# Optimization experiments

Hardware: AMD Instinct MI355X
Metric: run time of the kernel (lower is better)

The kernel has to match this reference:

```python
import jax, jax.numpy as jnp
import numpy as np

B, DIM, L = 16, 1024, 1024
EPS = 1e-12  # F.normalize eps


def l2norm(x, axis=1):
    # torch F.normalize: x / clamp_min(||x||_2, eps)
    n = jnp.sqrt(jnp.sum(x * x, axis=axis, keepdims=True))
    return x / jnp.maximum(n, EPS)


def setup_inputs() -> dict:
    key = jax.random.key(0)
    ks = jax.random.split(key, 8)
    inp = {
        "V": jax.random.normal(ks[0], (B, DIM, L), dtype=jnp.float32),
        "T": jax.random.normal(ks[1], (B, DIM, L), dtype=jnp.float32),
    }
    scale = 1.0 / np.sqrt(DIM)
    names = ["WQ1", "WK1", "WV1", "Wq2", "Wk2", "Wv2"]
    for i, nme in enumerate(names):
        inp[nme] = jax.random.normal(ks[2 + i], (DIM, DIM), dtype=jnp.float32) * scale
    return inp


def reference(V, T, WQ1, WK1, WV1, Wq2, Wk2, Wv2):
    # V, T: [B, dim, L]
    T = l2norm(T, axis=1)                      # normalize over feature dim
    Vt = jnp.swapaxes(V, -2, -1)               # [B, L, dim]
    Tt = jnp.swapaxes(T, -2, -1)               # [B, L, dim]

    relu = jax.nn.relu
    q1 = relu(jnp.einsum('bld,ed->ble', Vt, WQ1))
    k1 = relu(jnp.einsum('bld,ed->ble', Tt, WK1))
    v1 = relu(jnp.einsum('bld,ed->ble', Tt, WV1))
    q2 = relu(jnp.einsum('bld,ed->ble', Tt, Wq2))
    k2 = relu(jnp.einsum('bld,ed->ble', Vt, Wk2))
    v2 = relu(jnp.einsum('bld,ed->ble', Vt, Wv2))

    inv_sqrt_d = 1.0 / jnp.sqrt(jnp.asarray(DIM, dtype=q1.dtype))

    s1 = jnp.einsum('bqd,bkd->bqk', q1, k1) * inv_sqrt_d   # [B, Lv, Lt]
    p1 = jax.nn.softmax(s1, axis=1)                        # softmax over query axis (dim=1)
    w1 = jnp.einsum('bqk,bkd->bqd', p1, v1)                # [B, Lv, dim]
    cV = l2norm(V + jnp.swapaxes(w1, -2, -1), axis=1)      # [B, dim, Lv]

    s2 = jnp.einsum('bqd,bkd->bqk', q2, k2) * inv_sqrt_d   # [B, Lt, Lv]
    p2 = jax.nn.softmax(s2, axis=1)
    w2 = jnp.einsum('bqk,bkd->bqd', p2, v2)                # [B, Lt, dim]
    cT = l2norm(T + jnp.swapaxes(w2, -2, -1), axis=1)      # [B, dim, Lt]

    return l2norm(cV + cT, axis=1)
```

## Files before the change

kernel.cpp:

```cpp
#include <hip/hip_runtime.h>

#define L 1024
#define DIM 1024
#define NB 16

typedef unsigned short u16;
typedef __attribute__((ext_vector_type(4))) float f32x4;
typedef __attribute__((ext_vector_type(8))) short s16x8;

__device__ __forceinline__ float bf2f(u16 x){
  union { unsigned u; float f; } c; c.u = ((unsigned)x) << 16; return c.f;
}
__device__ __forceinline__ u16 f2bf(float f){
  union { float f; unsigned u; } c; c.f = f;
  unsigned r = c.u + 0x7fffu + ((c.u >> 16) & 1u);
  return (u16)(r >> 16);
}
__device__ __forceinline__ void gload_lds16(const void* g, void* l){
  __builtin_amdgcn_global_load_lds(
      (const __attribute__((address_space(1))) void*)g,
      (__attribute__((address_space(3))) void*)l, 16, 0, 0);
}

struct WPtrs { const float* p[6]; };

__global__ __launch_bounds__(256) void k_wconv(WPtrs wp, u16* out){
  long idx = (long)blockIdx.x * blockDim.x + threadIdx.x;
  long base = idx * 4;
  int w = (int)(base >> 20);
  long off = base & ((1 << 20) - 1);
  float4 v = *(const float4*)(wp.p[w] + off);
  ushort4 o;
  o.x = f2bf(v.x); o.y = f2bf(v.y); o.z = f2bf(v.z); o.w = f2bf(v.w);
  *(ushort4*)(out + base) = o;
}

__global__ __launch_bounds__(256) void k_transpose(const float* X, u16* Xt, int bo){
  __shared__ u16 tile[64][68];
  int b = blockIdx.y;
  int d0 = (blockIdx.x >> 4) * 64;
  int l0 = (blockIdx.x & 15) * 64;
  const float* Xb = X + (long)(bo + b) * DIM * L;
  u16* Xtb = Xt + (long)b * L * DIM;
  int q = threadIdx.x & 15, g = threadIdx.x >> 4;
  for (int r = g; r < 64; r += 16){
    float4 v = *(const float4*)(Xb + (long)(d0 + r) * L + l0 + q * 4);
    ushort4 h; h.x = f2bf(v.x); h.y = f2bf(v.y); h.z = f2bf(v.z); h.w = f2bf(v.w);
    *(ushort4*)&tile[r][q * 4] = h;
  }
  __syncthreads();
  for (int r = g; r < 64; r += 16){
    ushort4 h;
    h.x = tile[q * 4 + 0][r]; h.y = tile[q * 4 + 1][r];
    h.z = tile[q * 4 + 2][r]; h.w = tile[q * 4 + 3][r];
    *(ushort4*)&Xtb[(long)(l0 + r) * DIM + d0 + q * 4] = h;
  }
}

__global__ __launch_bounds__(256) void k_tnorm(const float* T_, u16* Tnt, float* rT, int bo){
  __shared__ float red[16][16][5];
  __shared__ float rn[64];
  __shared__ u16 tile[64][68];
  int b = blockIdx.y; int l0 = blockIdx.x * 64;
  const float* Tb = T_ + (long)(bo + b) * DIM * L;
  int q = threadIdx.x & 15, g = threadIdx.x >> 4;
  f32x4 ss = {0.f, 0.f, 0.f, 0.f};
  for (int d = g; d < DIM; d += 16){
    float4 v = *(const float4*)(Tb + (long)d * L + l0 + q * 4);
    f32x4 vv = {v.x, v.y, v.z, v.w};
    ss += vv * vv;
  }
  #pragma unroll
  for (int e = 0; e < 4; e++) red[g][q][e] = ss[e];
  __syncthreads();
  if (threadIdx.x < 64){
    int c = threadIdx.x;
    float n = 0.f;
    #pragma unroll
    for (int gg = 0; gg < 16; gg++) n += red[gg][c >> 2][c & 3];
    float r = 1.0f / fmaxf(sqrtf(n), 1e-12f);
    rn[c] = r;
    rT[(long)b * L + l0 + c] = r;
  }
  __syncthreads();
  float r0 = rn[q * 4], r1 = rn[q * 4 + 1], r2 = rn[q * 4 + 2], r3 = rn[q * 4 + 3];
  u16* Tntb = Tnt + (long)b * L * DIM;
  for (int ch = 0; ch < 16; ch++){
    int dbase = ch * 64;
    for (int r = g; r < 64; r += 16){
      float4 v = *(const float4*)(Tb + (long)(dbase + r) * L + l0 + q * 4);
      ushort4 h;
      h.x = f2bf(v.x * r0); h.y = f2bf(v.y * r1);
      h.z = f2bf(v.z * r2); h.w = f2bf(v.w * r3);
      *(ushort4*)&tile[r][q * 4] = h;
    }
    __syncthreads();
    for (int r = g; r < 64; r += 16){
      ushort4 h;
      h.x = tile[q * 4 + 0][r]; h.y = tile[q * 4 + 1][r];
      h.z = tile[q * 4 + 2][r]; h.w = tile[q * 4 + 3][r];
      *(ushort4*)&Tntb[(long)(l0 + r) * DIM + dbase + q * 4] = h;
    }
    __syncthreads();
  }
}


struct GemmDesc {
  const u16* A[4]; const u16* B[4]; u16* C[4];
  long sA[4], sB[4], sC[4];
  int epi[4];
  float scale;
};

#define PH(slot, mq, nq, LA, LB, STAGE, WAITC) do {                           \
  if (LA){                                                                    \
    _Pragma("unroll")                                                         \
    for (int f = 0; f < 4; f++){                                              \
      av[f][0] = *(const s16x8*)&lds[(slot)*16384 + arow + (mq)*4096 + f*1024 + cko0]; \
      av[f][1] = *(const s16x8*)&lds[(slot)*16384 + arow + (mq)*4096 + f*1024 + cko1]; \
    }                                                                         \
  }                                                                           \
  if (LB){                                                                    \
    _Pragma("unroll")                                                         \
    for (int g2 = 0; g2 < 2; g2++){                                           \
      bv[nq][g2][0] = *(const s16x8*)&lds[32768 + (slot)*16384 + brow + (nq)*2048 + g2*1024 + cko0]; \
      bv[nq][g2][1] = *(const s16x8*)&lds[32768 + (slot)*16384 + brow + (nq)*2048 + g2*1024 + cko1]; \
    }                                                                         \
  }                                                                           \
  STAGE;                                                                      \
  WAITC;                                                                      \
  __builtin_amdgcn_s_barrier();                                               \
  asm volatile("s_waitcnt lgkmcnt(0)" ::: "memory");                          \
  __builtin_amdgcn_sched_barrier(0);                                          \
  __builtin_amdgcn_s_setprio(1);                                              \
  _Pragma("unroll")                                                           \
  for (int f = 0; f < 4; f++)                                                 \
    _Pragma("unroll")                                                         \
    for (int g2 = 0; g2 < 2; g2++){                                           \
      acc[(mq)*4+f][(nq)*2+g2] = __builtin_amdgcn_mfma_f32_16x16x32_bf16(     \
          av[f][0], bv[nq][g2][0], acc[(mq)*4+f][(nq)*2+g2], 0, 0, 0);        \
      acc[(mq)*4+f][(nq)*2+g2] = __builtin_amdgcn_mfma_f32_16x16x32_bf16(     \
          av[f][1], bv[nq][g2][1], acc[(mq)*4+f][(nq)*2+g2], 0, 0, 0);        \
    }                                                                         \
  __builtin_amdgcn_s_setprio(0);                                              \
  __builtin_amdgcn_s_barrier();                                               \
} while(0)

__global__ __launch_bounds__(512, 2) void k_gemmM(GemmDesc gd, int shift){
  constexpr int K = 1024, NN = 1024, NT = K / 64, NIT = NT / 2;
  __shared__ u16 lds[65536];

  int tid = threadIdx.x;
  int w = tid >> 6, l = tid & 63;
  int wr = w >> 2, wc = w & 3;
  int lr = l & 15, cb = l >> 4;

  int nwg = gridDim.x, cpx = nwg >> 3;
  int swz = (blockIdx.x & 7) * cpx + (blockIdx.x >> 3);
  int mat = swz >> shift;
  int local = swz & ((1 << shift) - 1);
  int batch = local >> 4;
  int tile = local & 15;
  int bm = (tile >> 2) * 256, bn = (tile & 3) * 256;

  const u16* Ab = gd.A[mat] + (long)batch * gd.sA[mat] + (long)bm * K;
  const u16* Bb = gd.B[mat] + (long)batch * gd.sB[mat] + (long)bn * K;
  int epi = gd.epi[mat];

  int arow = (wr * 128 + lr) * 64;
  int brow = (wc * 64 + lr) * 64;
  int cko0 = ((cb) ^ (lr & 7)) * 8;
  int cko1 = ((4 + cb) ^ (lr & 7)) * 8;

  int srow8 = l >> 3;
  int schunk = (l & 7) ^ (l >> 3);

  auto stA = [&](int slot, int t, int q){
    #pragma unroll
    for (int j = 0; j < 2; j++){
      int wb = w * 2 + j;
      int gr = ((wb >> 3) * 128) + ((wb & 7) * 8) + q * 64;
      gload_lds16(Ab + (long)(gr + srow8) * K + t * 64 + schunk * 8,
                  (u16*)lds + slot * 16384 + gr * 64);
    }
  };
  auto stB = [&](int slot, int t, int q){
    #pragma unroll
    for (int j = 0; j < 2; j++){
      int wb = w * 2 + j;
      int gr = ((wb >> 2) * 64) + ((wb & 3) * 8) + q * 32;
      gload_lds16(Bb + (long)(gr + srow8) * K + t * 64 + schunk * 8,
                  (u16*)lds + 32768 + slot * 16384 + gr * 64);
    }
  };

  f32x4 acc[8][4] = {};
  s16x8 av[4][2];
  s16x8 bv[2][2][2];

  stA(0, 0, 0); stB(0, 0, 0); stA(0, 0, 1); stB(0, 0, 1);
  stA(1, 1, 0); stB(1, 1, 0);
  asm volatile("s_waitcnt vmcnt(4)" ::: "memory");
  __builtin_amdgcn_s_barrier();

  #pragma unroll 1
  for (int i = 0; i < NIT - 1; ++i){
    int t1 = 2 * i + 1, t2 = 2 * i + 2, t3 = 2 * i + 3;
    PH(0, 0, 0, 1, 1, stA(1, t1, 1), (void)0);
    PH(0, 0, 1, 0, 1, stB(1, t1, 1), (void)0);
    PH(0, 1, 0, 1, 0, stA(0, t2, 0), (void)0);
    PH(0, 1, 1, 0, 0, stB(0, t2, 0), asm volatile("s_waitcnt vmcnt(4)" ::: "memory"));
    PH(1, 0, 0, 1, 1, stA(0, t2, 1), (void)0);
    PH(1, 0, 1, 0, 1, stB(0, t2, 1), (void)0);
    PH(1, 1, 0, 1, 0, stA(1, t3, 0), (void)0);
    PH(1, 1, 1, 0, 0, stB(1, t3, 0), asm volatile("s_waitcnt vmcnt(4)" ::: "memory"));
  }
  {
    int t1 = NT - 1;
    PH(0, 0, 0, 1, 1, stA(1, t1, 1), (void)0);
    PH(0, 0, 1, 0, 1, stB(1, t1, 1), (void)0);
    PH(0, 1, 0, 1, 0, (void)0, (void)0);
    PH(0, 1, 1, 0, 0, (void)0, asm volatile("s_waitcnt vmcnt(0)" ::: "memory"));
    PH(1, 0, 0, 1, 1, (void)0, (void)0);
    PH(1, 0, 1, 0, 1, (void)0, (void)0);
    PH(1, 1, 0, 1, 0, (void)0, (void)0);
    PH(1, 1, 1, 0, 0, (void)0, (void)0);
  }

  u16* Cb = gd.C[mat] + (long)batch * gd.sC[mat];
  float sc = gd.scale;
  int cb4 = cb * 4;
  #pragma unroll
  for (int ai = 0; ai < 8; ai++)
    #pragma unroll
    for (int j = 0; j < 4; j++)
      #pragma unroll
      for (int r = 0; r < 4; r++){
        float v = acc[ai][j][r];
        if (epi == 0) v = fmaxf(v, 0.f);
        else if (epi == 1) v = __expf(v * sc);
        int row = bm + wr * 128 + ai * 16 + cb4 + r;
        int col = bn + wc * 64 + j * 16 + lr;
        Cb[(long)row * NN + col] = f2bf(v);
      }
}

__global__ __launch_bounds__(256) void k_colsum(const u16* E1, const u16* E2,
                                                float* iz1, float* iz2){
  __shared__ float red[32][8][9];
  int side = blockIdx.x >> 4;
  int k0 = (blockIdx.x & 15) * 64;
  int b = blockIdx.y;
  const u16* Eb = (side ? E2 : E1) + (long)b * L * L + k0;
  float* izp = (side ? iz2 : iz1) + (long)b * L + k0;
  int co = threadIdx.x & 7, g = threadIdx.x >> 3;
  float z[8] = {0.f, 0.f, 0.f, 0.f, 0.f, 0.f, 0.f, 0.f};
  for (int qq = g; qq < L; qq += 32){
    s16x8 h = *(const s16x8*)(Eb + (long)qq * L + co * 8);
    #pragma unroll
    for (int e = 0; e < 8; e++) z[e] += bf2f((u16)h[e]);
  }
  #pragma unroll
  for (int e = 0; e < 8; e++) red[g][co][e] = z[e];
  __syncthreads();
  if (threadIdx.x < 64){
    int c = threadIdx.x;
    float s = 0.f;
    #pragma unroll
    for (int gg = 0; gg < 32; gg++) s += red[gg][c >> 3][c & 7];
    izp[c] = 1.0f / s;
  }
}

__global__ __launch_bounds__(256) void k_zapply(u16* v1, u16* v2,
                                                const float* iz1, const float* iz2){
  int side = blockIdx.y;
  u16* v = side ? v2 : v1;
  const float* izp = side ? iz2 : iz1;
  long base = ((long)blockIdx.x * 256 + threadIdx.x) * 8;
  int batch = (int)(base >> 20);
  int k = (int)(base & 1023);
  s16x8 h = *(const s16x8*)(v + base);
  const float* z = izp + (long)batch * 1024 + k;
  float4 z0 = *(const float4*)z;
  float4 z1 = *(const float4*)(z + 4);
  s16x8 o;
  o[0] = (short)f2bf(bf2f((u16)h[0]) * z0.x);
  o[1] = (short)f2bf(bf2f((u16)h[1]) * z0.y);
  o[2] = (short)f2bf(bf2f((u16)h[2]) * z0.z);
  o[3] = (short)f2bf(bf2f((u16)h[3]) * z0.w);
  o[4] = (short)f2bf(bf2f((u16)h[4]) * z1.x);
  o[5] = (short)f2bf(bf2f((u16)h[5]) * z1.y);
  o[6] = (short)f2bf(bf2f((u16)h[6]) * z1.z);
  o[7] = (short)f2bf(bf2f((u16)h[7]) * z1.w);
  *(s16x8*)(v + base) = o;
}

__global__ __launch_bounds__(1024) void k_final(const float* V, const float* T_,
                                                const float* rT, const u16* w1t,
                                                const u16* w2t, float* out, int bo){
  __shared__ float red[64][16][13];
  __shared__ float fac[3][64];
  int b = blockIdx.y;
  int c0 = blockIdx.x * 64;
  long gbase = (long)(bo + b) * DIM * L + c0;
  long lbase = (long)b * DIM * L + c0;
  int cq = threadIdx.x & 15, g = threadIdx.x >> 4;
  int coff = cq * 4;
  float4 rt4 = *(const float4*)(rT + (long)b * L + c0 + coff);
  f32x4 rtv = {rt4.x, rt4.y, rt4.z, rt4.w};
  f32x4 s1 = {0.f,0.f,0.f,0.f}, s2 = {0.f,0.f,0.f,0.f}, s12 = {0.f,0.f,0.f,0.f};
  for (int d = g; d < DIM; d += 64){
    long o = (long)d * L + coff;
    float4 v = *(const float4*)(V + gbase + o);
    float4 t = *(const float4*)(T_ + gbase + o);
    ushort4 w1 = *(const ushort4*)(w1t + lbase + o);
    ushort4 w2 = *(const ushort4*)(w2t + lbase + o);
    f32x4 a = {v.x + bf2f(w1.x), v.y + bf2f(w1.y), v.z + bf2f(w1.z), v.w + bf2f(w1.w)};
    f32x4 tt = {t.x, t.y, t.z, t.w};
    f32x4 bb = tt * rtv;
    bb[0] += bf2f(w2.x); bb[1] += bf2f(w2.y); bb[2] += bf2f(w2.z); bb[3] += bf2f(w2.w);
    s1 += a * a; s2 += bb * bb; s12 += a * bb;
  }
  #pragma unroll
  for (int e = 0; e < 4; e++){
    red[g][cq][e] = s1[e];
    red[g][cq][4 + e] = s2[e];
    red[g][cq][8 + e] = s12[e];
  }
  __syncthreads();
  if (threadIdx.x < 192){
    int q = threadIdx.x / 12, s = threadIdx.x % 12;
    float acc = 0.f;
    #pragma unroll 8
    for (int gg = 0; gg < 64; gg++) acc += red[gg][q][s];
    red[0][q][s] = acc;
  }
  __syncthreads();
  if (threadIdx.x < 64){
    int c = threadIdx.x;
    float n1 = red[0][c >> 2][c & 3];
    float n2 = red[0][c >> 2][4 + (c & 3)];
    float cc = red[0][c >> 2][8 + (c & 3)];
    float rn1 = 1.f / fmaxf(sqrtf(n1), 1e-12f);
    float rn2 = 1.f / fmaxf(sqrtf(n2), 1e-12f);
    float n3 = n1 * rn1 * rn1 + 2.f * cc * rn1 * rn2 + n2 * rn2 * rn2;
    float rn3 = 1.f / fmaxf(sqrtf(n3), 1e-12f);
    fac[0][c] = rn1; fac[1][c] = rn2; fac[2][c] = rn3;
  }
  __syncthreads();
  f32x4 f1, f2, f3;
  #pragma unroll
  for (int e = 0; e < 4; e++){
    f1[e] = fac[0][coff + e]; f2[e] = fac[1][coff + e]; f3[e] = fac[2][coff + e];
  }
  for (int d = g; d < DIM; d += 64){
    long o = (long)d * L + coff;
    float4 v = *(const float4*)(V + gbase + o);
    float4 t = *(const float4*)(T_ + gbase + o);
    ushort4 w1 = *(const ushort4*)(w1t + lbase + o);
    ushort4 w2 = *(const ushort4*)(w2t + lbase + o);
    f32x4 a = {v.x + bf2f(w1.x), v.y + bf2f(w1.y), v.z + bf2f(w1.z), v.w + bf2f(w1.w)};
    f32x4 tt = {t.x, t.y, t.z, t.w};
    f32x4 bb = tt * rtv;
    bb[0] += bf2f(w2.x); bb[1] += bf2f(w2.y); bb[2] += bf2f(w2.z); bb[3] += bf2f(w2.w);
    f32x4 r = (a * f1 + bb * f2) * f3;
    float4 st = {r[0], r[1], r[2], r[3]};
    *(float4*)(out + gbase + o) = st;
  }
}

extern "C" void kernel_launch(void* const* d_in, const int* in_sizes, int n_in,
                              void* d_out, int out_size, void* d_ws, size_t ws_size,
                              hipStream_t stream) {
  const float* V = (const float*)d_in[0];
  const float* T = (const float*)d_in[1];
  char* ws = (char*)d_ws;
  const long MB = 1 << 20;
  float* out = (float*)d_out;

  int G = NB;
  while (G > 1 && (size_t)((13 + 24 * (long)G) * MB) > ws_size) G >>= 1;
  int shift = 4 + (31 - __builtin_clz((unsigned)G));

  u16*   Wb  = (u16*)(ws);
  float* rT  = (float*)(ws + 12 * MB);
  float* iz1 = (float*)(ws + 12 * MB + 256 * 1024);
  float* iz2 = (float*)(ws + 12 * MB + 512 * 1024);
  char*  bufs = ws + 13 * MB;
  long   BUF  = (long)G * 2 * MB;
  u16* Vt  = (u16*)(bufs + 0  * BUF);
  u16* Tnt = (u16*)(bufs + 1  * BUF);
  u16* q1  = (u16*)(bufs + 2  * BUF);
  u16* k1  = (u16*)(bufs + 3  * BUF);
  u16* q2  = (u16*)(bufs + 4  * BUF);
  u16* k2  = (u16*)(bufs + 5  * BUF);
  u16* E1  = (u16*)(bufs + 6  * BUF);
  u16* E2  = (u16*)(bufs + 7  * BUF);
  u16* v1  = (u16*)(bufs + 8  * BUF);
  u16* v2  = (u16*)(bufs + 9  * BUF);
  u16* w1b = (u16*)(bufs + 10 * BUF);
  u16* w2b = (u16*)(bufs + 11 * BUF);

  WPtrs wp;
  for (int i = 0; i < 6; i++) wp.p[i] = (const float*)d_in[2 + i];
  const u16* WQ1 = Wb + 0L * MB; const u16* WK1 = Wb + 1L * MB;
  const u16* WV1 = Wb + 2L * MB; const u16* Wq2 = Wb + 3L * MB;
  const u16* Wk2 = Wb + 4L * MB; const u16* Wv2 = Wb + 5L * MB;

  long LD = (long)L * DIM;
  const float invsq = 0.03125f;

  GemmDesc g1;
  g1.A[0] = Vt;  g1.B[0] = WQ1; g1.C[0] = q1;
  g1.A[1] = Tnt; g1.B[1] = WK1; g1.C[1] = k1;
  g1.A[2] = Tnt; g1.B[2] = Wq2; g1.C[2] = q2;
  g1.A[3] = Vt;  g1.B[3] = Wk2; g1.C[3] = k2;
  for (int i = 0; i < 4; i++){ g1.sA[i] = LD; g1.sB[i] = 0; g1.sC[i] = LD; g1.epi[i] = 0; }
  g1.scale = 0.f;

  GemmDesc g2;
  g2.A[0] = q1;  g2.B[0] = k1;  g2.C[0] = E1; g2.sA[0] = LD; g2.sB[0] = LD; g2.sC[0] = LD; g2.epi[0] = 1;
  g2.A[1] = q2;  g2.B[1] = k2;  g2.C[1] = E2; g2.sA[1] = LD; g2.sB[1] = LD; g2.sC[1] = LD; g2.epi[1] = 1;
  g2.A[2] = WV1; g2.B[2] = Tnt; g2.C[2] = v1; g2.sA[2] = 0;  g2.sB[2] = LD; g2.sC[2] = LD; g2.epi[2] = 0;
  g2.A[3] = Wv2; g2.B[3] = Vt;  g2.C[3] = v2; g2.sA[3] = 0;  g2.sB[3] = LD; g2.sC[3] = LD; g2.epi[3] = 0;
  g2.scale = invsq;

  GemmDesc g3;
  g3.A[0] = v1; g3.B[0] = E1; g3.C[0] = w1b;
  g3.A[1] = v2; g3.B[1] = E2; g3.C[1] = w2b;
  g3.A[2] = v1; g3.B[2] = E1; g3.C[2] = w1b;
  g3.A[3] = v1; g3.B[3] = E1; g3.C[3] = w1b;
  for (int i = 0; i < 4; i++){ g3.sA[i] = LD; g3.sB[i] = LD; g3.sC[i] = LD; g3.epi[i] = 3; }
  g3.scale = 0.f;

  k_wconv<<<6144, 256, 0, stream>>>(wp, Wb);

  for (int bo = 0; bo < NB; bo += G){
    k_transpose<<<dim3(256, G), 256, 0, stream>>>(V, Vt, bo);
    k_tnorm<<<dim3(16, G), 256, 0, stream>>>(T, Tnt, rT, bo);

    k_gemmM<<<4 * 16 * G, 512, 0, stream>>>(g1, shift);
    k_gemmM<<<4 * 16 * G, 512, 0, stream>>>(g2, shift);
    k_colsum<<<dim3(32, G), 256, 0, stream>>>(E1, E2, iz1, iz2);
    k_zapply<<<dim3(G * 512, 2), 256, 0, stream>>>(v1, v2, iz1, iz2);
    k_gemmM<<<2 * 16 * G, 512, 0, stream>>>(g3, shift);

    k_final<<<dim3(16, G), 1024, 0, stream>>>(V, T, rT, w1b, w2b, out, bo);
  }
}
```

Measured before the change: 654.5 us.

## Reuse workspace buffers via liveness aliasing and fuse column-sum with value scaling

Replaces the twelve per-batch workspace buffers with seven aliased slots. GEMM launches are regrouped (T-side projections, then V-side projections, then each score GEMM alone) so that dead buffers can be overwritten, which lets a larger batch group G fit in the workspace. The column-sum kernel now also rescales v1/v2 by the inverse sums, removing the separate zapply launch and its global round trip for the inverse sums. The final kernel's loops are unrolled by 4. In exchange there are more, smaller GEMM launches, and correctness depends on the aliasing order being right.

```diff
diff --git a/kernel.cpp b/kernel.cpp
--- a/kernel.cpp
+++ b/kernel.cpp
@@ -246,14 +246,15 @@
       }
 }
 
-__global__ __launch_bounds__(256) void k_colsum(const u16* E1, const u16* E2,
-                                                float* iz1, float* iz2){
+__global__ __launch_bounds__(256) void k_colzs(const u16* E1, const u16* E2,
+                                               u16* v1, u16* v2){
   __shared__ float red[32][8][9];
+  __shared__ float invs[64];
   int side = blockIdx.x >> 4;
   int k0 = (blockIdx.x & 15) * 64;
   int b = blockIdx.y;
   const u16* Eb = (side ? E2 : E1) + (long)b * L * L + k0;
-  float* izp = (side ? iz2 : iz1) + (long)b * L + k0;
+  u16* vb = (side ? v2 : v1) + (long)b * L * DIM + k0;
   int co = threadIdx.x & 7, g = threadIdx.x >> 3;
   float z[8] = {0.f, 0.f, 0.f, 0.f, 0.f, 0.f, 0.f, 0.f};
   for (int qq = g; qq < L; qq += 32){
@@ -269,32 +270,19 @@
     float s = 0.f;
     #pragma unroll
     for (int gg = 0; gg < 32; gg++) s += red[gg][c >> 3][c & 7];
-    izp[c] = 1.0f / s;
-  }
-}
-
-__global__ __launch_bounds__(256) void k_zapply(u16* v1, u16* v2,
-                                                const float* iz1, const float* iz2){
-  int side = blockIdx.y;
-  u16* v = side ? v2 : v1;
-  const float* izp = side ? iz2 : iz1;
-  long base = ((long)blockIdx.x * 256 + threadIdx.x) * 8;
-  int batch = (int)(base >> 20);
-  int k = (int)(base & 1023);
-  s16x8 h = *(const s16x8*)(v + base);
-  const float* z = izp + (long)batch * 1024 + k;
-  float4 z0 = *(const float4*)z;
-  float4 z1 = *(const float4*)(z + 4);
-  s16x8 o;
-  o[0] = (short)f2bf(bf2f((u16)h[0]) * z0.x);
-  o[1] = (short)f2bf(bf2f((u16)h[1]) * z0.y);
-  o[2] = (short)f2bf(bf2f((u16)h[2]) * z0.z);
-  o[3] = (short)f2bf(bf2f((u16)h[3]) * z0.w);
-  o[4] = (short)f2bf(bf2f((u16)h[4]) * z1.x);
-  o[5] = (short)f2bf(bf2f((u16)h[5]) * z1.y);
-  o[6] = (short)f2bf(bf2f((u16)h[6]) * z1.z);
-  o[7] = (short)f2bf(bf2f((u16)h[7]) * z1.w);
-  *(s16x8*)(v + base) = o;
+    invs[c] = 1.0f / s;
+  }
+  __syncthreads();
+  float iz[8];
+  #pragma unroll
+  for (int e = 0; e < 8; e++) iz[e] = invs[co * 8 + e];
+  for (int r = g; r < DIM; r += 32){
+    s16x8 h = *(const s16x8*)(vb + (long)r * L + co * 8);
+    s16x8 o;
+    #pragma unroll
+    for (int e = 0; e < 8; e++) o[e] = (short)f2bf(bf2f((u16)h[e]) * iz[e]);
+    *(s16x8*)(vb + (long)r * L + co * 8) = o;
+  }
 }
 
 __global__ __launch_bounds__(1024) void k_final(const float* V, const float* T_,
@@ -311,6 +299,7 @@
   float4 rt4 = *(const float4*)(rT + (long)b * L + c0 + coff);
   f32x4 rtv = {rt4.x, rt4.y, rt4.z, rt4.w};
   f32x4 s1 = {0.f,0.f,0.f,0.f}, s2 = {0.f,0.f,0.f,0.f}, s12 = {0.f,0.f,0.f,0.f};
+  #pragma unroll 4
   for (int d = g; d < DIM; d += 64){
     long o = (long)d * L + coff;
     float4 v = *(const float4*)(V + gbase + o);
@@ -355,6 +344,7 @@
   for (int e = 0; e < 4; e++){
     f1[e] = fac[0][coff + e]; f2[e] = fac[1][coff + e]; f3[e] = fac[2][coff + e];
   }
+  #pragma unroll 4
   for (int d = g; d < DIM; d += 64){
     long o = (long)d * L + coff;
     float4 v = *(const float4*)(V + gbase + o);
@@ -381,27 +371,20 @@
   float* out = (float*)d_out;
 
   int G = NB;
-  while (G > 1 && (size_t)((13 + 24 * (long)G) * MB) > ws_size) G >>= 1;
+  while (G > 1 && (size_t)((13 + 14 * (long)G) * MB) > ws_size) G >>= 1;
   int shift = 4 + (31 - __builtin_clz((unsigned)G));
 
   u16*   Wb  = (u16*)(ws);
   float* rT  = (float*)(ws + 12 * MB);
-  float* iz1 = (float*)(ws + 12 * MB + 256 * 1024);
-  float* iz2 = (float*)(ws + 12 * MB + 512 * 1024);
   char*  bufs = ws + 13 * MB;
   long   BUF  = (long)G * 2 * MB;
-  u16* Vt  = (u16*)(bufs + 0  * BUF);
-  u16* Tnt = (u16*)(bufs + 1  * BUF);
-  u16* q1  = (u16*)(bufs + 2  * BUF);
-  u16* k1  = (u16*)(bufs + 3  * BUF);
-  u16* q2  = (u16*)(bufs + 4  * BUF);
-  u16* k2  = (u16*)(bufs + 5  * BUF);
-  u16* E1  = (u16*)(bufs + 6  * BUF);
-  u16* E2  = (u16*)(bufs + 7  * BUF);
-  u16* v1  = (u16*)(bufs + 8  * BUF);
-  u16* v2  = (u16*)(bufs + 9  * BUF);
-  u16* w1b = (u16*)(bufs + 10 * BUF);
-  u16* w2b = (u16*)(bufs + 11 * BUF);
+  u16* S0 = (u16*)(bufs + 0 * BUF);
+  u16* S1 = (u16*)(bufs + 1 * BUF);
+  u16* S2 = (u16*)(bufs + 2 * BUF);
+  u16* S3 = (u16*)(bufs + 3 * BUF);
+  u16* S4 = (u16*)(bufs + 4 * BUF);
+  u16* S5 = (u16*)(bufs + 5 * BUF);
+  u16* S6 = (u16*)(bufs + 6 * BUF);
 
   WPtrs wp;
   for (int i = 0; i < 6; i++) wp.p[i] = (const float*)d_in[2 + i];
@@ -412,28 +395,42 @@
   long LD = (long)L * DIM;
   const float invsq = 0.03125f;
 
-  GemmDesc g1;
-  g1.A[0] = Vt;  g1.B[0] = WQ1; g1.C[0] = q1;
-  g1.A[1] = Tnt; g1.B[1] = WK1; g1.C[1] = k1;
-  g1.A[2] = Tnt; g1.B[2] = Wq2; g1.C[2] = q2;
-  g1.A[3] = Vt;  g1.B[3] = Wk2; g1.C[3] = k2;
-  for (int i = 0; i < 4; i++){ g1.sA[i] = LD; g1.sB[i] = 0; g1.sC[i] = LD; g1.epi[i] = 0; }
-  g1.scale = 0.f;
-
-  GemmDesc g2;
-  g2.A[0] = q1;  g2.B[0] = k1;  g2.C[0] = E1; g2.sA[0] = LD; g2.sB[0] = LD; g2.sC[0] = LD; g2.epi[0] = 1;
-  g2.A[1] = q2;  g2.B[1] = k2;  g2.C[1] = E2; g2.sA[1] = LD; g2.sB[1] = LD; g2.sC[1] = LD; g2.epi[1] = 1;
-  g2.A[2] = WV1; g2.B[2] = Tnt; g2.C[2] = v1; g2.sA[2] = 0;  g2.sB[2] = LD; g2.sC[2] = LD; g2.epi[2] = 0;
-  g2.A[3] = Wv2; g2.B[3] = Vt;  g2.C[3] = v2; g2.sA[3] = 0;  g2.sB[3] = LD; g2.sC[3] = LD; g2.epi[3] = 0;
-  g2.scale = invsq;
-
-  GemmDesc g3;
-  g3.A[0] = v1; g3.B[0] = E1; g3.C[0] = w1b;
-  g3.A[1] = v2; g3.B[1] = E2; g3.C[1] = w2b;
-  g3.A[2] = v1; g3.B[2] = E1; g3.C[2] = w1b;
-  g3.A[3] = v1; g3.B[3] = E1; g3.C[3] = w1b;
-  for (int i = 0; i < 4; i++){ g3.sA[i] = LD; g3.sB[i] = LD; g3.sC[i] = LD; g3.epi[i] = 3; }
-  g3.scale = 0.f;
+  u16* Vt = S0, *Tnt = S1;
+  u16* k1 = S2, *v1 = S3, *q2 = S4;
+  u16* q1 = S5, *k2 = S6, *v2 = S1;
+  u16* E1 = S0, *E2 = S5;
+  u16* w1b = S2, *w2b = S4;
+
+  GemmDesc g1 = {};
+  g1.A[0] = Tnt; g1.B[0] = WK1; g1.C[0] = k1; g1.sA[0] = LD; g1.sB[0] = 0;  g1.sC[0] = LD;
+  g1.A[1] = WV1; g1.B[1] = Tnt; g1.C[1] = v1; g1.sA[1] = 0;  g1.sB[1] = LD; g1.sC[1] = LD;
+  g1.A[2] = Tnt; g1.B[2] = Wq2; g1.C[2] = q2; g1.sA[2] = LD; g1.sB[2] = 0;  g1.sC[2] = LD;
+  g1.epi[0] = g1.epi[1] = g1.epi[2] = 0; g1.scale = 0.f;
+  g1.A[3] = Tnt; g1.B[3] = WK1; g1.C[3] = k1; g1.sA[3] = LD; g1.sB[3] = 0; g1.sC[3] = LD; g1.epi[3] = 0;
+
+  GemmDesc g2 = {};
+  g2.A[0] = Vt;  g2.B[0] = WQ1; g2.C[0] = q1; g2.sA[0] = LD; g2.sB[0] = 0;  g2.sC[0] = LD;
+  g2.A[1] = Vt;  g2.B[1] = Wk2; g2.C[1] = k2; g2.sA[1] = LD; g2.sB[1] = 0;  g2.sC[1] = LD;
+  g2.A[2] = Wv2; g2.B[2] = Vt;  g2.C[2] = v2; g2.sA[2] = 0;  g2.sB[2] = LD; g2.sC[2] = LD;
+  g2.epi[0] = g2.epi[1] = g2.epi[2] = 0; g2.scale = 0.f;
+  g2.A[3] = Vt; g2.B[3] = WQ1; g2.C[3] = q1; g2.sA[3] = LD; g2.sB[3] = 0; g2.sC[3] = LD; g2.epi[3] = 0;
+
+  GemmDesc g3a = {};
+  g3a.A[0] = q1; g3a.B[0] = k1; g3a.C[0] = E1;
+  g3a.sA[0] = LD; g3a.sB[0] = LD; g3a.sC[0] = LD; g3a.epi[0] = 1; g3a.scale = invsq;
+  for (int i = 1; i < 4; i++){ g3a.A[i] = q1; g3a.B[i] = k1; g3a.C[i] = E1;
+    g3a.sA[i] = LD; g3a.sB[i] = LD; g3a.sC[i] = LD; g3a.epi[i] = 1; }
+
+  GemmDesc g3b = g3a;
+  for (int i = 0; i < 4; i++){ g3b.A[i] = q2; g3b.B[i] = k2; g3b.C[i] = E2; }
+
+  GemmDesc g4 = {};
+  g4.A[0] = v1; g4.B[0] = E1; g4.C[0] = w1b;
+  g4.A[1] = v2; g4.B[1] = E2; g4.C[1] = w2b;
+  g4.A[2] = v1; g4.B[2] = E1; g4.C[2] = w1b;
+  g4.A[3] = v1; g4.B[3] = E1; g4.C[3] = w1b;
+  for (int i = 0; i < 4; i++){ g4.sA[i] = LD; g4.sB[i] = LD; g4.sC[i] = LD; g4.epi[i] = 3; }
+  g4.scale = 0.f;
 
   k_wconv<<<6144, 256, 0, stream>>>(wp, Wb);
 
@@ -441,11 +438,12 @@
     k_transpose<<<dim3(256, G), 256, 0, stream>>>(V, Vt, bo);
     k_tnorm<<<dim3(16, G), 256, 0, stream>>>(T, Tnt, rT, bo);
 
-    k_gemmM<<<4 * 16 * G, 512, 0, stream>>>(g1, shift);
-    k_gemmM<<<4 * 16 * G, 512, 0, stream>>>(g2, shift);
-    k_colsum<<<dim3(32, G), 256, 0, stream>>>(E1, E2, iz1, iz2);
-    k_zapply<<<dim3(G * 512, 2), 256, 0, stream>>>(v1, v2, iz1, iz2);
-    k_gemmM<<<2 * 16 * G, 512, 0, stream>>>(g3, shift);
+    k_gemmM<<<3 * 16 * G, 512, 0, stream>>>(g1, shift);
+    k_gemmM<<<3 * 16 * G, 512, 0, stream>>>(g2, shift);
+    k_gemmM<<<1 * 16 * G, 512, 0, stream>>>(g3a, shift);
+    k_gemmM<<<1 * 16 * G, 512, 0, stream>>>(g3b, shift);
+    k_colzs<<<dim3(32, G), 256, 0, stream>>>(E1, E2, v1, v2);
+    k_gemmM<<<2 * 16 * G, 512, 0, stream>>>(g4, shift);
 
     k_final<<<dim3(16, G), 1024, 0, stream>>>(V, T, rT, w1b, w2b, out, bo);
   }
```

Result: faster. 591.4 us (-9.6%).
